# Optimization experiments

Hardware: AMD Instinct MI355X
Metric: run time of the kernel (lower is better)

## Reference

```python
import jax, jax.numpy as jnp
import numpy as np

H = 1024  # hidden_size


def setup_inputs() -> dict:
    key = jax.random.key(0)
    k1, k2, k3, k4, k5, k6 = jax.random.split(key, 6)
    B, T = 32, 2048
    bound_attn = 1.0 / np.sqrt(2 * H)  # nn.Linear default init bound
    bound_v = 1.0 / np.sqrt(H)
    return {
        "encoder_outputs": jax.random.normal(k1, (B, T, H), dtype=jnp.float32),
        "hidden": jax.random.normal(k2, (B, H), dtype=jnp.float32),
        "W_attn": jax.random.uniform(k3, (H, 2 * H), minval=-bound_attn, maxval=bound_attn, dtype=jnp.float32),
        "b_attn": jax.random.uniform(k4, (H,), minval=-bound_attn, maxval=bound_attn, dtype=jnp.float32),
        "W_v": jax.random.uniform(k5, (1, H), minval=-bound_v, maxval=bound_v, dtype=jnp.float32),
        "b_v": jax.random.uniform(k6, (1,), minval=-bound_v, maxval=bound_v, dtype=jnp.float32),
    }


def reference(encoder_outputs, hidden, W_attn, b_attn, W_v, b_v):
    # score(h, e) = v(attn(cat(h, e))) — split attn weight over the concat axis:
    # W_attn = [Wh | We], each [H, H]
    Wh = W_attn[:, :H]
    We = W_attn[:, H:]
    # energy: [B, T, H] = hidden@Wh^T (broadcast over T) + enc@We^T + b
    energy = (jnp.einsum("bh,kh->bk", hidden, Wh)[:, None, :]
              + jnp.einsum("bth,kh->btk", encoder_outputs, We)
              + b_attn)
    # attn_energies: [B, T]
    scores = jnp.einsum("btk,ok->bto", energy, W_v)[..., 0] + b_v[0]
    attention_weights = jax.nn.softmax(scores, axis=1)  # softmax over T
    # context: [B, H] = weights bmm encoder_outputs, then squeeze
    context = jnp.einsum("bt,bth->bh", attention_weights, encoder_outputs)
    return context
```

## Files before the change

### kernel.cpp

```cpp
#include <hip/hip_runtime.h>
#include <math.h>

#define HH   1024
#define TT   2048
#define BB   32
#define NC   16
#define TC   (TT / NC)
#define NTH  256
#define TUN  4

__global__ __launch_bounds__(NTH) void compute_v_kernel(
    const float* __restrict__ W_attn, const float* __restrict__ W_v,
    float* __restrict__ v_out)
{
    const int h = blockIdx.x * NTH + threadIdx.x;
    const float* col = W_attn + HH + h;
    float s = 0.f;
#pragma unroll 8
    for (int k = 0; k < HH; ++k)
        s = fmaf(W_v[k], col[(size_t)k * (2 * HH)], s);
    v_out[h] = s;
}

__global__ __launch_bounds__(NTH) void attn_pass_kernel(
    const float* __restrict__ enc, const float* __restrict__ v,
    float* __restrict__ ws_m, float* __restrict__ ws_l,
    float* __restrict__ ws_acc)
{
    const int c    = blockIdx.x;
    const int b    = blockIdx.y;
    const int tid  = threadIdx.x;
    const int lane = tid & 63;
    const int wave = tid >> 6;

    const float4 v4 = reinterpret_cast<const float4*>(v)[tid];
    const float4* enc4 = reinterpret_cast<const float4*>(enc)
                         + ((size_t)b * TT + (size_t)c * TC) * (HH / 4);

    __shared__ float red[TUN][4];

    float  m = -INFINITY;
    float  l = 0.f;
    float4 acc = make_float4(0.f, 0.f, 0.f, 0.f);

    for (int t0 = 0; t0 < TC; t0 += TUN) {
        float4 e[TUN];
        float  p[TUN];
#pragma unroll
        for (int i = 0; i < TUN; ++i)
            e[i] = enc4[(size_t)(t0 + i) * (HH / 4) + tid];

#pragma unroll
        for (int i = 0; i < TUN; ++i) {
            p[i] = e[i].x * v4.x + e[i].y * v4.y + e[i].z * v4.z + e[i].w * v4.w;
#pragma unroll
            for (int off = 32; off > 0; off >>= 1)
                p[i] += __shfl_down(p[i], off, 64);
        }
        if (lane == 0) {
#pragma unroll
            for (int i = 0; i < TUN; ++i) red[i][wave] = p[i];
        }
        __syncthreads();

        float s[TUN];
        float mn = m;
#pragma unroll
        for (int i = 0; i < TUN; ++i) {
            s[i] = red[i][0] + red[i][1] + red[i][2] + red[i][3];
            mn = fmaxf(mn, s[i]);
        }
        __syncthreads();

        const float alpha = __expf(m - mn);
        float w[TUN];
        float wsum = 0.f;
#pragma unroll
        for (int i = 0; i < TUN; ++i) { w[i] = __expf(s[i] - mn); wsum += w[i]; }

        l = l * alpha + wsum;
        acc.x *= alpha; acc.y *= alpha; acc.z *= alpha; acc.w *= alpha;
#pragma unroll
        for (int i = 0; i < TUN; ++i) {
            acc.x = fmaf(w[i], e[i].x, acc.x);
            acc.y = fmaf(w[i], e[i].y, acc.y);
            acc.z = fmaf(w[i], e[i].z, acc.z);
            acc.w = fmaf(w[i], e[i].w, acc.w);
        }
        m = mn;
    }

    const int idx = b * NC + c;
    if (tid == 0) { ws_m[idx] = m; ws_l[idx] = l; }
    reinterpret_cast<float4*>(ws_acc + (size_t)idx * HH)[tid] = acc;
}

__global__ __launch_bounds__(NTH) void combine_kernel(
    const float* __restrict__ ws_m, const float* __restrict__ ws_l,
    const float* __restrict__ ws_acc, float* __restrict__ out)
{
    const int b   = blockIdx.x;
    const int tid = threadIdx.x;

    float M = -INFINITY;
#pragma unroll
    for (int c = 0; c < NC; ++c) M = fmaxf(M, ws_m[b * NC + c]);

    float sc[NC];
    float L = 0.f;
#pragma unroll
    for (int c = 0; c < NC; ++c) {
        sc[c] = __expf(ws_m[b * NC + c] - M);
        L = fmaf(sc[c], ws_l[b * NC + c], L);
    }

    float4 r = make_float4(0.f, 0.f, 0.f, 0.f);
#pragma unroll
    for (int c = 0; c < NC; ++c) {
        const float4 a =
            reinterpret_cast<const float4*>(ws_acc + (size_t)(b * NC + c) * HH)[tid];
        r.x = fmaf(sc[c], a.x, r.x);
        r.y = fmaf(sc[c], a.y, r.y);
        r.z = fmaf(sc[c], a.z, r.z);
        r.w = fmaf(sc[c], a.w, r.w);
    }
    const float inv = 1.f / L;
    reinterpret_cast<float4*>(out + (size_t)b * HH)[tid] =
        make_float4(r.x * inv, r.y * inv, r.z * inv, r.w * inv);
}

extern "C" void kernel_launch(void* const* d_in, const int* in_sizes, int n_in,
                              void* d_out, int out_size, void* d_ws, size_t ws_size,
                              hipStream_t stream) {
    const float* enc    = (const float*)d_in[0];
    const float* W_attn = (const float*)d_in[2];
    const float* W_v    = (const float*)d_in[4];
    float* out = (float*)d_out;

    float* ws     = (float*)d_ws;
    float* v      = ws;
    float* ws_m   = ws + 1024;
    float* ws_l   = ws + 1536;
    float* ws_acc = ws + 2048;

    compute_v_kernel<<<HH / NTH, NTH, 0, stream>>>(W_attn, W_v, v);
    attn_pass_kernel<<<dim3(NC, BB), NTH, 0, stream>>>(enc, v, ws_m, ws_l, ws_acc);
    combine_kernel<<<BB, NTH, 0, stream>>>(ws_m, ws_l, ws_acc, out);
}
```

Before: 445.4 us.

## Split v computation over K, give each wave its own time rows with prefetch

The v-vector GEMV is split across 16 K-slices with a separate reduction kernel, so it uses more blocks than the previous 4-block launch. The attention pass now gives each wave its own contiguous run of timesteps and reduces the dot product within the wave. This removes the two per-step block barriers, and the next row is register-prefetched. Chunks double to 32 and the wave partials are merged through shared memory, at the cost of an extra launch, more registers and more workspace traffic.

```diff
diff --git a/kernel.cpp b/kernel.cpp
--- a/kernel.cpp
+++ b/kernel.cpp
@@ -4,21 +4,35 @@
 #define HH   1024
 #define TT   2048
 #define BB   32
-#define NC   16
+#define NC   32
 #define TC   (TT / NC)
-#define NTH  256
-#define TUN  4
+#define NWV  4
+#define TPW  (TC / NWV)
+#define NTH  (NWV * 64)
+#define KSL  16
 
-__global__ __launch_bounds__(NTH) void compute_v_kernel(
+__global__ __launch_bounds__(256) void compute_v_part(
     const float* __restrict__ W_attn, const float* __restrict__ W_v,
-    float* __restrict__ v_out)
+    float* __restrict__ vpart)
 {
-    const int h = blockIdx.x * NTH + threadIdx.x;
+    const int h  = blockIdx.x * 256 + threadIdx.x;
+    const int ks = blockIdx.y;
+    const int k0 = ks * (HH / KSL);
     const float* col = W_attn + HH + h;
     float s = 0.f;
 #pragma unroll 8
-    for (int k = 0; k < HH; ++k)
+    for (int k = k0; k < k0 + HH / KSL; ++k)
         s = fmaf(W_v[k], col[(size_t)k * (2 * HH)], s);
+    vpart[ks * HH + h] = s;
+}
+
+__global__ __launch_bounds__(256) void compute_v_reduce(
+    const float* __restrict__ vpart, float* __restrict__ v_out)
+{
+    const int h = blockIdx.x * 256 + threadIdx.x;
+    float s = 0.f;
+#pragma unroll
+    for (int ks = 0; ks < KSL; ++ks) s += vpart[ks * HH + h];
     v_out[h] = s;
 }
 
@@ -33,69 +47,100 @@
     const int lane = tid & 63;
     const int wave = tid >> 6;
 
-    const float4 v4 = reinterpret_cast<const float4*>(v)[tid];
+    float4 v4[4];
+#pragma unroll
+    for (int j = 0; j < 4; ++j)
+        v4[j] = reinterpret_cast<const float4*>(v)[lane + 64 * j];
+
+    const int t0 = c * TC + wave * TPW;
     const float4* enc4 = reinterpret_cast<const float4*>(enc)
-                         + ((size_t)b * TT + (size_t)c * TC) * (HH / 4);
-
-    __shared__ float red[TUN][4];
+                         + ((size_t)b * TT + t0) * (HH / 4);
 
     float  m = -INFINITY;
     float  l = 0.f;
-    float4 acc = make_float4(0.f, 0.f, 0.f, 0.f);
+    float4 acc[4] = {make_float4(0,0,0,0), make_float4(0,0,0,0),
+                     make_float4(0,0,0,0), make_float4(0,0,0,0)};
 
-    for (int t0 = 0; t0 < TC; t0 += TUN) {
-        float4 e[TUN];
-        float  p[TUN];
+    float4 e[4];
 #pragma unroll
-        for (int i = 0; i < TUN; ++i)
-            e[i] = enc4[(size_t)(t0 + i) * (HH / 4) + tid];
+    for (int j = 0; j < 4; ++j) e[j] = enc4[lane + 64 * j];
+
+    for (int i = 0; i < TPW; ++i) {
+        float4 en[4];
+        const bool more = (i + 1 < TPW);
+        if (more) {
+#pragma unroll
+            for (int j = 0; j < 4; ++j)
+                en[j] = enc4[(size_t)(i + 1) * (HH / 4) + lane + 64 * j];
+        }
+        float p = 0.f;
+#pragma unroll
+        for (int j = 0; j < 4; ++j) {
+            p = fmaf(e[j].x, v4[j].x, p);
+            p = fmaf(e[j].y, v4[j].y, p);
+            p = fmaf(e[j].z, v4[j].z, p);
+            p = fmaf(e[j].w, v4[j].w, p);
+        }
+#pragma unroll
+        for (int off = 1; off < 64; off <<= 1)
+            p += __shfl_xor(p, off, 64);
+
+        const float mn    = fmaxf(m, p);
+        const float alpha = __expf(m - mn);
+        const float w     = __expf(p - mn);
+        l = fmaf(l, alpha, w);
+#pragma unroll
+        for (int j = 0; j < 4; ++j) {
+            acc[j].x = fmaf(acc[j].x, alpha, w * e[j].x);
+            acc[j].y = fmaf(acc[j].y, alpha, w * e[j].y);
+            acc[j].z = fmaf(acc[j].z, alpha, w * e[j].z);
+            acc[j].w = fmaf(acc[j].w, alpha, w * e[j].w);
+        }
+        m = mn;
+        if (more) {
+#pragma unroll
+            for (int j = 0; j < 4; ++j) e[j] = en[j];
+        }
+    }
+
+    __shared__ float sm[NWV], sl[NWV];
+    __shared__ float4 sacc[NWV * 256];
+
+    if (lane == 0) { sm[wave] = m; sl[wave] = l; }
+    __syncthreads();
+
+    float M = -INFINITY;
+#pragma unroll
+    for (int w2 = 0; w2 < NWV; ++w2) M = fmaxf(M, sm[w2]);
+    const float myscale = __expf(m - M);
 
 #pragma unroll
-        for (int i = 0; i < TUN; ++i) {
-            p[i] = e[i].x * v4.x + e[i].y * v4.y + e[i].z * v4.z + e[i].w * v4.w;
+    for (int j = 0; j < 4; ++j) {
+        float4 a = acc[j];
+        a.x *= myscale; a.y *= myscale; a.z *= myscale; a.w *= myscale;
+        sacc[wave * 256 + lane + 64 * j] = a;
+    }
+    __syncthreads();
+
+    float4 r = make_float4(0, 0, 0, 0);
 #pragma unroll
-            for (int off = 32; off > 0; off >>= 1)
-                p[i] += __shfl_down(p[i], off, 64);
-        }
-        if (lane == 0) {
-#pragma unroll
-            for (int i = 0; i < TUN; ++i) red[i][wave] = p[i];
-        }
-        __syncthreads();
-
-        float s[TUN];
-        float mn = m;
-#pragma unroll
-        for (int i = 0; i < TUN; ++i) {
-            s[i] = red[i][0] + red[i][1] + red[i][2] + red[i][3];
-            mn = fmaxf(mn, s[i]);
-        }
-        __syncthreads();
-
-        const float alpha = __expf(m - mn);
-        float w[TUN];
-        float wsum = 0.f;
-#pragma unroll
-        for (int i = 0; i < TUN; ++i) { w[i] = __expf(s[i] - mn); wsum += w[i]; }
-
-        l = l * alpha + wsum;
-        acc.x *= alpha; acc.y *= alpha; acc.z *= alpha; acc.w *= alpha;
-#pragma unroll
-        for (int i = 0; i < TUN; ++i) {
-            acc.x = fmaf(w[i], e[i].x, acc.x);
-            acc.y = fmaf(w[i], e[i].y, acc.y);
-            acc.z = fmaf(w[i], e[i].z, acc.z);
-            acc.w = fmaf(w[i], e[i].w, acc.w);
-        }
-        m = mn;
+    for (int w2 = 0; w2 < NWV; ++w2) {
+        const float4 a = sacc[w2 * 256 + tid];
+        r.x += a.x; r.y += a.y; r.z += a.z; r.w += a.w;
     }
 
     const int idx = b * NC + c;
-    if (tid == 0) { ws_m[idx] = m; ws_l[idx] = l; }
-    reinterpret_cast<float4*>(ws_acc + (size_t)idx * HH)[tid] = acc;
+    reinterpret_cast<float4*>(ws_acc + (size_t)idx * HH)[tid] = r;
+    if (tid == 0) {
+        float L = 0.f;
+#pragma unroll
+        for (int w2 = 0; w2 < NWV; ++w2) L = fmaf(sl[w2], __expf(sm[w2] - M), L);
+        ws_m[idx] = M;
+        ws_l[idx] = L;
+    }
 }
 
-__global__ __launch_bounds__(NTH) void combine_kernel(
+__global__ __launch_bounds__(256) void combine_kernel(
     const float* __restrict__ ws_m, const float* __restrict__ ws_l,
     const float* __restrict__ ws_acc, float* __restrict__ out)
 {
@@ -106,23 +151,18 @@
 #pragma unroll
     for (int c = 0; c < NC; ++c) M = fmaxf(M, ws_m[b * NC + c]);
 
-    float sc[NC];
     float L = 0.f;
+    float4 r = make_float4(0, 0, 0, 0);
 #pragma unroll
     for (int c = 0; c < NC; ++c) {
-        sc[c] = __expf(ws_m[b * NC + c] - M);
-        L = fmaf(sc[c], ws_l[b * NC + c], L);
-    }
-
-    float4 r = make_float4(0.f, 0.f, 0.f, 0.f);
-#pragma unroll
-    for (int c = 0; c < NC; ++c) {
+        const float sc = __expf(ws_m[b * NC + c] - M);
+        L = fmaf(sc, ws_l[b * NC + c], L);
         const float4 a =
             reinterpret_cast<const float4*>(ws_acc + (size_t)(b * NC + c) * HH)[tid];
-        r.x = fmaf(sc[c], a.x, r.x);
-        r.y = fmaf(sc[c], a.y, r.y);
-        r.z = fmaf(sc[c], a.z, r.z);
-        r.w = fmaf(sc[c], a.w, r.w);
+        r.x = fmaf(sc, a.x, r.x);
+        r.y = fmaf(sc, a.y, r.y);
+        r.z = fmaf(sc, a.z, r.z);
+        r.w = fmaf(sc, a.w, r.w);
     }
     const float inv = 1.f / L;
     reinterpret_cast<float4*>(out + (size_t)b * HH)[tid] =
@@ -139,11 +179,13 @@
 
     float* ws     = (float*)d_ws;
     float* v      = ws;
-    float* ws_m   = ws + 1024;
-    float* ws_l   = ws + 1536;
-    float* ws_acc = ws + 2048;
+    float* vpart  = ws + 1024;
+    float* ws_m   = ws + 1024 + KSL * HH;
+    float* ws_l   = ws_m + BB * NC;
+    float* ws_acc = ws_l + BB * NC;
 
-    compute_v_kernel<<<HH / NTH, NTH, 0, stream>>>(W_attn, W_v, v);
+    compute_v_part<<<dim3(4, KSL), 256, 0, stream>>>(W_attn, W_v, vpart);
+    compute_v_reduce<<<HH / 256, 256, 0, stream>>>(vpart, v);
     attn_pass_kernel<<<dim3(NC, BB), NTH, 0, stream>>>(enc, v, ws_m, ws_l, ws_acc);
-    combine_kernel<<<BB, NTH, 0, stream>>>(ws_m, ws_l, ws_acc, out);
+    combine_kernel<<<BB, 256, 0, stream>>>(ws_m, ws_l, ws_acc, out);
 }
```

New measurement: 380.3 us. 1.17x faster.
